# Kernel tuning notes

Measured on AMD Instinct MI355X. Metric: run time of the kernel, lower is better.

Reference implementation:

```python
import jax, jax.numpy as jnp
import numpy as np

IMG_H, IMG_W = 800, 1344
STRIDE = 16
FH, FW = IMG_H // STRIDE, IMG_W // STRIDE  # 50, 84
C = 1024
N_PROP = 3000
K_KEEP = 512          # post-NMS proposals kept by merge_proposals
POOL = 14             # C4 ROI-align output resolution
NMS_THRESH = 0.7
NUM_CLASSES = 80


def _make_boxes(key, n):
    r = jax.random.uniform(key, (n, 4))
    cx = r[:, 0] * IMG_W
    cy = r[:, 1] * IMG_H
    w = 16.0 + r[:, 2] * 480.0
    h = 16.0 + r[:, 3] * 480.0
    x0 = jnp.clip(cx - w / 2, 0.0, IMG_W)
    y0 = jnp.clip(cy - h / 2, 0.0, IMG_H)
    x1 = jnp.clip(cx + w / 2, 0.0, IMG_W)
    y1 = jnp.clip(cy + h / 2, 0.0, IMG_H)
    return jnp.stack([x0, y0, x1, y1], axis=-1)


def setup_inputs() -> dict:
    key = jax.random.key(0)
    ks = jax.random.split(key, 14)
    feat = jax.random.normal(ks[0], (C, FH, FW), jnp.float32)
    boxes1 = _make_boxes(ks[1], N_PROP)
    boxes2 = _make_boxes(ks[2], N_PROP)
    logits1 = jax.random.normal(ks[3], (N_PROP,), jnp.float32)
    logits2 = jax.random.normal(ks[4], (N_PROP,), jnp.float32)
    levels1 = jnp.zeros((N_PROP,), jnp.int32)  # single C4 level
    levels2 = jnp.zeros((N_PROP,), jnp.int32)
    scale1 = 1.0 + 0.02 * jax.random.normal(ks[5], (C,), jnp.float32)
    bias1 = 0.02 * jax.random.normal(ks[6], (C,), jnp.float32)
    scale2 = 1.0 + 0.02 * jax.random.normal(ks[7], (C,), jnp.float32)
    bias2 = 0.02 * jax.random.normal(ks[8], (C,), jnp.float32)
    W_cls1 = 0.01 * jax.random.normal(ks[9], (C, NUM_CLASSES + 1), jnp.float32)
    b_cls1 = jnp.zeros((NUM_CLASSES + 1,), jnp.float32)
    W_box1 = 0.001 * jax.random.normal(ks[10], (C, NUM_CLASSES * 4), jnp.float32)
    b_box1 = jnp.zeros((NUM_CLASSES * 4,), jnp.float32)
    W_cls2 = 0.01 * jax.random.normal(ks[11], (C, NUM_CLASSES + 1), jnp.float32)
    b_cls2 = jnp.zeros((NUM_CLASSES + 1,), jnp.float32)
    W_box2 = 0.001 * jax.random.normal(ks[12], (C, NUM_CLASSES * 4), jnp.float32)
    b_box2 = jnp.zeros((NUM_CLASSES * 4,), jnp.float32)
    return dict(feat=feat, boxes1=boxes1, boxes2=boxes2, logits1=logits1,
                logits2=logits2, levels1=levels1, levels2=levels2,
                scale1=scale1, bias1=bias1, scale2=scale2, bias2=bias2,
                W_cls1=W_cls1, b_cls1=b_cls1, W_box1=W_box1, b_box1=b_box1,
                W_cls2=W_cls2, b_cls2=b_cls2, W_box2=W_box2, b_box2=b_box2)


def _clip_boxes(boxes):
    return jnp.stack([jnp.clip(boxes[:, 0], 0.0, IMG_W),
                      jnp.clip(boxes[:, 1], 0.0, IMG_H),
                      jnp.clip(boxes[:, 2], 0.0, IMG_W),
                      jnp.clip(boxes[:, 3], 0.0, IMG_H)], axis=-1)


def _nms(boxes, scores, k, thresh):
    """Greedy NMS; returns k kept indices (fixed-size, jit-friendly)."""
    areas = (boxes[:, 2] - boxes[:, 0]) * (boxes[:, 3] - boxes[:, 1])

    def body(i, state):
        sw, keep = state
        idx = jnp.argmax(sw)
        keep = keep.at[i].set(idx.astype(jnp.int32))
        b = boxes[idx]
        ix0 = jnp.maximum(b[0], boxes[:, 0])
        iy0 = jnp.maximum(b[1], boxes[:, 1])
        ix1 = jnp.minimum(b[2], boxes[:, 2])
        iy1 = jnp.minimum(b[3], boxes[:, 3])
        inter = jnp.maximum(ix1 - ix0, 0.0) * jnp.maximum(iy1 - iy0, 0.0)
        iou = inter / (areas[idx] + areas - inter + 1e-9)
        sw = jnp.where(iou > thresh, -jnp.inf, sw)
        sw = sw.at[idx].set(-jnp.inf)
        return sw, keep

    keep0 = jnp.zeros((k,), jnp.int32)
    _, keep = jax.lax.fori_loop(0, k, body, (scores, keep0))
    return keep


def _roi_align(feat, boxes, spatial_scale, pool):
    """ROIAlign (aligned=True, sampling_ratio=1). feat [C,H,W], boxes [R,4] -> [R,C,pool,pool]."""
    Cc, H, W = feat.shape
    b = boxes * spatial_scale - 0.5
    x0, y0, x1, y1 = b[:, 0], b[:, 1], b[:, 2], b[:, 3]
    bw = (x1 - x0) / pool
    bh = (y1 - y0) / pool
    grid = jnp.arange(pool, dtype=feat.dtype) + 0.5
    xs = x0[:, None] + grid[None, :] * bw[:, None]  # [R,P]
    ys = y0[:, None] + grid[None, :] * bh[:, None]  # [R,P]
    yf = jnp.floor(ys); xf = jnp.floor(xs)
    ly = ys - yf; lx = xs - xf
    y0c = jnp.clip(yf.astype(jnp.int32), 0, H - 1)
    y1c = jnp.clip(yf.astype(jnp.int32) + 1, 0, H - 1)
    x0c = jnp.clip(xf.astype(jnp.int32), 0, W - 1)
    x1c = jnp.clip(xf.astype(jnp.int32) + 1, 0, W - 1)

    def g(Y, X):  # gather -> [C,R,P,P]
        return feat[:, Y[:, :, None], X[:, None, :]]

    wy0 = (1.0 - ly); wy1 = ly  # [R,P]
    wx0 = (1.0 - lx); wx1 = lx
    out = (g(y0c, x0c) * (wy0[:, :, None] * wx0[:, None, :])
           + g(y0c, x1c) * (wy0[:, :, None] * wx1[:, None, :])
           + g(y1c, x0c) * (wy1[:, :, None] * wx0[:, None, :])
           + g(y1c, x1c) * (wy1[:, :, None] * wx1[:, None, :]))
    return jnp.transpose(out, (1, 0, 2, 3))  # [R,C,P,P]


def _box_head(roi_feats, scale, bias, W_cls, b_cls, W_box, b_box):
    bf = roi_feats * scale[None, :, None, None] + bias[None, :, None, None]
    x = bf.mean(axis=(2, 3))  # [R,C]
    return bf, x @ W_cls + b_cls, x @ W_box + b_box


def reference(feat, boxes1, boxes2, logits1, logits2, levels1, levels2,
              scale1, bias1, scale2, bias2,
              W_cls1, b_cls1, W_box1, b_box1,
              W_cls2, b_cls2, W_box2, b_box2):
    boxes = _clip_boxes(jnp.concatenate([boxes1, boxes2], axis=0))
    scores = jnp.concatenate([logits1, logits2], axis=0)
    levels = jnp.concatenate([levels1, levels2], axis=0)
    # batched_nms level-offset trick (all zeros for single C4 level)
    off = levels.astype(boxes.dtype)[:, None] * float(max(IMG_H, IMG_W) + 1)
    keep = _nms(boxes + off, scores, K_KEEP, NMS_THRESH)
    prop = boxes[keep]  # [K,4] merged proposals

    roi = _roi_align(feat, prop, 1.0 / STRIDE, POOL)  # [K,C,P,P]
    bf1, s1, d1 = _box_head(roi, scale1, bias1, W_cls1, b_cls1, W_box1, b_box1)
    bf2, s2, d2 = _box_head(roi, scale2, bias2, W_cls2, b_cls2, W_box2, b_box2)
    return (bf1, bf2, s1, s2, d1, prop, feat)
```

## Files before the change

kernel.cpp:

```cpp
#include <hip/hip_runtime.h>

#define FHH 50
#define FWW 84
#define HW 4200
#define NBOX 6000
#define NPAD 6144
#define KKEEP 512
#define WSTRIDE 192

#define OFF_BF1  0ULL
#define OFF_BF2  102760448ULL
#define OFF_S1   205520896ULL
#define OFF_S2   205562368ULL
#define OFF_D1   205603840ULL
#define OFF_PROP 205767680ULL
#define OFF_FEAT 205769728ULL

__global__ __launch_bounds__(256) void k_transpose(const float* __restrict__ feat,
                                                   float* __restrict__ featT,
                                                   float* __restrict__ out_feat) {
  __shared__ float t[32][33];
  int hw0 = blockIdx.x * 32;
  int c0  = blockIdx.y * 32;
  int tx = threadIdx.x & 31, ty = threadIdx.x >> 5;
#pragma unroll
  for (int p = 0; p < 4; ++p) {
    int c = c0 + ty + p * 8;
    int hw = hw0 + tx;
    if (hw < HW) {
      float v = feat[(size_t)c * HW + hw];
      t[ty + p * 8][tx] = v;
      out_feat[(size_t)c * HW + hw] = v;
    }
  }
  __syncthreads();
#pragma unroll
  for (int p = 0; p < 4; ++p) {
    int hw = hw0 + ty + p * 8;
    int c = c0 + tx;
    if (hw < HW) featT[((size_t)hw << 10) + c] = t[tx][ty + p * 8];
  }
}

__global__ __launch_bounds__(256) void k_prep(const float4* __restrict__ boxes1,
                                              const float4* __restrict__ boxes2,
                                              const float* __restrict__ logits1,
                                              const float* __restrict__ logits2,
                                              const int* __restrict__ levels1,
                                              const int* __restrict__ levels2,
                                              float4* __restrict__ nbox,
                                              float* __restrict__ area,
                                              unsigned long long* __restrict__ keys,
                                              int* __restrict__ rank) {
  int i = blockIdx.x * 256 + threadIdx.x;
  if (i >= NPAD) return;
  if (i >= NBOX) { keys[i] = 0ULL; return; }
  rank[i] = 0;
  float4 b; float sc; int lv;
  if (i < 3000) { b = boxes1[i]; sc = logits1[i]; lv = levels1[i]; }
  else          { b = boxes2[i - 3000]; sc = logits2[i - 3000]; lv = levels2[i - 3000]; }
  float x0 = fminf(fmaxf(b.x, 0.f), 1344.f);
  float y0 = fminf(fmaxf(b.y, 0.f), 800.f);
  float x1 = fminf(fmaxf(b.z, 0.f), 1344.f);
  float y1 = fminf(fmaxf(b.w, 0.f), 800.f);
  float off = __fmul_rn((float)lv, 1345.0f);
  x0 = __fadd_rn(x0, off); y0 = __fadd_rn(y0, off);
  x1 = __fadd_rn(x1, off); y1 = __fadd_rn(y1, off);
  nbox[i] = make_float4(x0, y0, x1, y1);
  area[i] = __fmul_rn(__fsub_rn(x1, x0), __fsub_rn(y1, y0));
  unsigned u = __float_as_uint(sc);
  u = (u & 0x80000000u) ? ~u : (u | 0x80000000u);
  keys[i] = ((unsigned long long)u << 32) | (unsigned)(0xFFFFFFFFu - (unsigned)i);
}

__global__ __launch_bounds__(256) void k_rank(const unsigned long long* __restrict__ keys,
                                              int* __restrict__ rank) {
  __shared__ unsigned long long ks[1024];
  int jb = blockIdx.y;
  for (int t = threadIdx.x; t < 1024; t += 256) ks[t] = keys[jb * 1024 + t];
  __syncthreads();
  int i = blockIdx.x * 256 + threadIdx.x;
  if (i >= NBOX) return;
  unsigned long long ki = keys[i];
  int c = 0;
  for (int j = 0; j < 1024; ++j) c += (ks[j] > ki) ? 1 : 0;
  if (c) atomicAdd(&rank[i], c);
}

__global__ __launch_bounds__(256) void k_scatter(const float4* __restrict__ nbox,
                                                 const float* __restrict__ area,
                                                 const int* __restrict__ rank,
                                                 float4* __restrict__ sboxes,
                                                 float* __restrict__ sarea,
                                                 int* __restrict__ sorig) {
  int i = blockIdx.x * 256 + threadIdx.x;
  if (i >= NBOX) return;
  int r = rank[i];
  sboxes[r] = nbox[i];
  sarea[r] = area[i];
  sorig[r] = i;
}

__global__ __launch_bounds__(192) void k_mask(const float4* __restrict__ sboxes,
                                              const float* __restrict__ sarea,
                                              unsigned* __restrict__ mask) {
  int i0 = blockIdx.x * 4;
  int w = threadIdx.x;
  float4 b0 = sboxes[i0 + 0], b1 = sboxes[i0 + 1], b2 = sboxes[i0 + 2], b3 = sboxes[i0 + 3];
  float a0 = sarea[i0 + 0], a1 = sarea[i0 + 1], a2 = sarea[i0 + 2], a3 = sarea[i0 + 3];
  unsigned m0 = 0, m1 = 0, m2 = 0, m3 = 0;
  int jbase = w * 32;
  for (int bb = 0; bb < 32; ++bb) {
    int j = jbase + bb;
    if (j >= NBOX) break;
    float4 bj = sboxes[j];
    float aj = sarea[j];
#define IOU_BIT(BR, AR, MR)                                                          \
    {                                                                                \
      float ix0 = fmaxf(BR.x, bj.x), iy0 = fmaxf(BR.y, bj.y);                        \
      float ix1 = fminf(BR.z, bj.z), iy1 = fminf(BR.w, bj.w);                        \
      float iw = fmaxf(__fsub_rn(ix1, ix0), 0.f), ih = fmaxf(__fsub_rn(iy1, iy0), 0.f); \
      float inter = __fmul_rn(iw, ih);                                               \
      float den = __fadd_rn(__fsub_rn(__fadd_rn(AR, aj), inter), 1e-9f);             \
      float iou = __fdiv_rn(inter, den);                                             \
      if (iou > 0.7f) MR |= (1u << bb);                                              \
    }
    IOU_BIT(b0, a0, m0) IOU_BIT(b1, a1, m1) IOU_BIT(b2, a2, m2) IOU_BIT(b3, a3, m3)
#undef IOU_BIT
  }
  mask[(size_t)(i0 + 0) * WSTRIDE + w] = m0;
  mask[(size_t)(i0 + 1) * WSTRIDE + w] = m1;
  mask[(size_t)(i0 + 2) * WSTRIDE + w] = m2;
  mask[(size_t)(i0 + 3) * WSTRIDE + w] = m3;
}

#define SCAN_CH 64
__global__ __launch_bounds__(256) void k_scan(const unsigned* __restrict__ mask,
                                              const int* __restrict__ sorig,
                                              int* __restrict__ keep) {
  __shared__ unsigned srows[SCAN_CH * WSTRIDE];
  __shared__ unsigned rem[WSTRIDE];
  __shared__ int s_sorig[SCAN_CH];
  __shared__ int s_done;
  int tid = threadIdx.x;
  for (int i = tid; i < WSTRIDE; i += 256) rem[i] = 0;
  if (tid == 0) s_done = 0;
  __syncthreads();
  int kept = 0;
  for (int g = 0; g < 94; ++g) {
    int base = g * SCAN_CH;
    size_t gbase = (size_t)base * WSTRIDE;
    for (int idx = tid; idx < SCAN_CH * WSTRIDE; idx += 256) {
      size_t gi = gbase + idx;
      srows[idx] = (gi < (size_t)NBOX * WSTRIDE) ? mask[gi] : 0u;
    }
    if (tid < SCAN_CH) {
      int i = base + tid;
      s_sorig[tid] = (i < NBOX) ? sorig[i] : 0;
    }
    __syncthreads();
    if (tid < 64) {
      int lane = tid;
      for (int ww = 0; ww < 2; ++ww) {
        int w = (base >> 5) + ww;
        int wbase = w * 32;
        unsigned valid;
        int nv = NBOX - wbase;
        valid = (nv <= 0) ? 0u : (nv >= 32 ? 0xFFFFFFFFu : ((1u << nv) - 1u));
        unsigned rw = rem[w];
        unsigned avail = ~rw & valid;
        while (avail && kept < KKEEP) {
          int b = __builtin_ctz(avail);
          int i = wbase + b;
          int rr = i - base;
          if (lane == 0) keep[kept] = s_sorig[rr];
          kept++;
          rem[lane]       |= srows[rr * WSTRIDE + lane];
          rem[64 + lane]  |= srows[rr * WSTRIDE + 64 + lane];
          rem[128 + lane] |= srows[rr * WSTRIDE + 128 + lane];
          rw = rem[w];
          unsigned gt = (b == 31) ? 0u : ~((2u << b) - 1u);
          avail = ~rw & valid & gt;
        }
        if (kept >= KKEEP) break;
      }
      if (lane == 0 && kept >= KKEEP) s_done = 1;
    }
    __syncthreads();
    if (s_done) break;
  }
  if (tid < 64) {
    for (int k = kept + tid; k < KKEEP; k += 64) keep[k] = 0;
  }
}

__global__ __launch_bounds__(256) void k_prop(const int* __restrict__ keep,
                                              const float4* __restrict__ boxes1,
                                              const float4* __restrict__ boxes2,
                                              float4* __restrict__ prop) {
  int k = blockIdx.x * 256 + threadIdx.x;
  if (k >= KKEEP) return;
  int o = keep[k];
  float4 b = (o < 3000) ? boxes1[o] : boxes2[o - 3000];
  prop[k] = make_float4(fminf(fmaxf(b.x, 0.f), 1344.f),
                        fminf(fmaxf(b.y, 0.f), 800.f),
                        fminf(fmaxf(b.z, 0.f), 1344.f),
                        fminf(fmaxf(b.w, 0.f), 800.f));
}

__global__ __launch_bounds__(256) void k_bilin(const float4* __restrict__ prop,
                                               float4* __restrict__ bilinW,
                                               int4* __restrict__ bilinA) {
  int r = blockIdx.x;
  int bin = threadIdx.x;
  if (bin >= 196) return;
  float4 pb = prop[r];
  const float ss = 0.0625f;
  float x0s = pb.x * ss - 0.5f, y0s = pb.y * ss - 0.5f;
  float bw = (pb.z * ss - 0.5f - x0s) / 14.0f;
  float bh = (pb.w * ss - 0.5f - y0s) / 14.0f;
  int py = bin / 14, px = bin - py * 14;
  float xs = x0s + ((float)px + 0.5f) * bw;
  float ys = y0s + ((float)py + 0.5f) * bh;
  float xf = floorf(xs), yf = floorf(ys);
  float lx = xs - xf, ly = ys - yf;
  int ix = (int)xf, iy = (int)yf;
  int x0c = min(max(ix, 0), FWW - 1), x1c = min(max(ix + 1, 0), FWW - 1);
  int y0c = min(max(iy, 0), FHH - 1), y1c = min(max(iy + 1, 0), FHH - 1);
  float wy0 = 1.f - ly, wx0 = 1.f - lx;
  bilinW[r * 196 + bin] = make_float4(wy0 * wx0, wy0 * lx, ly * wx0, ly * lx);
  bilinA[r * 196 + bin] = make_int4((y0c * FWW + x0c) << 10, (y0c * FWW + x1c) << 10,
                                    (y1c * FWW + x0c) << 10, (y1c * FWW + x1c) << 10);
}

__global__ __launch_bounds__(256) void k_roi(const float* __restrict__ featT,
                                             const float4* __restrict__ bilinW,
                                             const int4* __restrict__ bilinA,
                                             const float* __restrict__ scale1,
                                             const float* __restrict__ bias1,
                                             const float* __restrict__ scale2,
                                             const float* __restrict__ bias2,
                                             float* __restrict__ bf1,
                                             float* __restrict__ bf2,
                                             float* __restrict__ x1w,
                                             float* __restrict__ x2w) {
  __shared__ float tile[64 * 197];
  __shared__ float part2f[4 * 64];
  __shared__ float sc1[64], bi1[64], sc2[64], bi2[64];
  int bid = blockIdx.x;
  int r = (bid & 7) + ((bid >> 7) << 3);
  int c0 = ((bid >> 3) & 15) * 64;
  int tid = threadIdx.x;
  int l16 = tid & 15, bg = tid >> 4;
  if (tid < 64) {
    sc1[tid] = scale1[c0 + tid]; bi1[tid] = bias1[c0 + tid];
    sc2[tid] = scale2[c0 + tid]; bi2[tid] = bias2[c0 + tid];
  }
  const float* fTb = featT + c0 + l16 * 4;
  const float4* bW = bilinW + r * 196;
  const int4* bA = bilinA + r * 196;
  float4 acc = make_float4(0.f, 0.f, 0.f, 0.f);

#define ROI_BODY(BB)                                                              \
  {                                                                               \
    float4 w = bW[BB]; int4 a = bA[BB];                                           \
    float4 g00 = *(const float4*)(fTb + a.x);                                     \
    float4 g01 = *(const float4*)(fTb + a.y);                                     \
    float4 g10 = *(const float4*)(fTb + a.z);                                     \
    float4 g11 = *(const float4*)(fTb + a.w);                                     \
    float vx = g00.x * w.x + g01.x * w.y + g10.x * w.z + g11.x * w.w;             \
    float vy = g00.y * w.x + g01.y * w.y + g10.y * w.z + g11.y * w.w;             \
    float vz = g00.z * w.x + g01.z * w.y + g10.z * w.z + g11.z * w.w;             \
    float vw = g00.w * w.x + g01.w * w.y + g10.w * w.z + g11.w * w.w;             \
    acc.x += vx; acc.y += vy; acc.z += vz; acc.w += vw;                           \
    int tb = l16 * 788 + (BB);                                                    \
    tile[tb] = vx; tile[tb + 197] = vy; tile[tb + 394] = vz; tile[tb + 591] = vw; \
  }

  int bb = bg;
#pragma unroll 4
  for (int i = 0; i < 12; ++i, bb += 16) ROI_BODY(bb)
  if (bg < 4) ROI_BODY(192 + bg)
#undef ROI_BODY

  acc.x += __shfl_xor(acc.x, 16); acc.y += __shfl_xor(acc.y, 16);
  acc.z += __shfl_xor(acc.z, 16); acc.w += __shfl_xor(acc.w, 16);
  acc.x += __shfl_xor(acc.x, 32); acc.y += __shfl_xor(acc.y, 32);
  acc.z += __shfl_xor(acc.z, 32); acc.w += __shfl_xor(acc.w, 32);
  if ((tid & 63) < 16) {
    int wv = tid >> 6;
    part2f[wv * 64 + l16 * 4 + 0] = acc.x;
    part2f[wv * 64 + l16 * 4 + 1] = acc.y;
    part2f[wv * 64 + l16 * 4 + 2] = acc.z;
    part2f[wv * 64 + l16 * 4 + 3] = acc.w;
  }
  __syncthreads();
  if (tid < 64) {
    float m = ((part2f[tid] + part2f[64 + tid]) + part2f[128 + tid]) + part2f[192 + tid];
    m = m / 196.0f;
    x1w[((size_t)r << 10) + c0 + tid] = m * sc1[tid] + bi1[tid];
    x2w[((size_t)r << 10) + c0 + tid] = m * sc2[tid] + bi2[tid];
  }
  size_t ob = ((size_t)((r << 10) + c0)) * 196;
  for (int it = 0; it < 49; ++it) {
    int flat = tid + it * 256;
    unsigned cl = (unsigned)flat / 196u;
    int bin = flat - (int)cl * 196;
    float v = tile[cl * 197 + bin];
    bf1[ob + flat] = v * sc1[cl] + bi1[cl];
    bf2[ob + flat] = v * sc2[cl] + bi2[cl];
  }
}

__global__ __launch_bounds__(256) void k_gemm(const float* __restrict__ x1,
                                              const float* __restrict__ x2,
                                              const float* __restrict__ Wc1, const float* __restrict__ bc1,
                                              const float* __restrict__ Wb1, const float* __restrict__ bb1,
                                              const float* __restrict__ Wc2, const float* __restrict__ bc2,
                                              float* __restrict__ s1, float* __restrict__ d1,
                                              float* __restrict__ s2) {
  int z = blockIdx.z;
  const float* A; const float* W; const float* bias; float* out; int N;
  if (z == 0)      { A = x1; W = Wc1; bias = bc1; out = s1; N = 81; }
  else if (z == 1) { A = x1; W = Wb1; bias = bb1; out = d1; N = 320; }
  else             { A = x2; W = Wc2; bias = bc2; out = s2; N = 81; }
  int n0 = blockIdx.y * 32;
  if (n0 >= N) return;
  int m0 = blockIdx.x * 32;
  __shared__ float As[32][34];
  __shared__ float Bs[32][34];
  int tid = threadIdx.x;
  int tx = tid & 15, ty = tid >> 4;
  float acc00 = 0, acc01 = 0, acc10 = 0, acc11 = 0;
  for (int k0 = 0; k0 < 1024; k0 += 32) {
    int mm = tid >> 3, g = tid & 7;
    float4 av = *(const float4*)(A + (size_t)(m0 + mm) * 1024 + k0 + g * 4);
    As[g * 4 + 0][mm] = av.x; As[g * 4 + 1][mm] = av.y;
    As[g * 4 + 2][mm] = av.z; As[g * 4 + 3][mm] = av.w;
    int nn = tid & 31, kh = tid >> 5;
#pragma unroll
    for (int qq = 0; qq < 4; ++qq) {
      int kk = kh + 8 * qq;
      int n = n0 + nn;
      Bs[kk][nn] = (n < N) ? W[(size_t)(k0 + kk) * N + n] : 0.f;
    }
    __syncthreads();
#pragma unroll
    for (int kk = 0; kk < 32; ++kk) {
      float2 a = *(const float2*)&As[kk][2 * ty];
      float2 b = *(const float2*)&Bs[kk][2 * tx];
      acc00 += a.x * b.x; acc01 += a.x * b.y;
      acc10 += a.y * b.x; acc11 += a.y * b.y;
    }
    __syncthreads();
  }
  int m = m0 + 2 * ty, n = n0 + 2 * tx;
  if (n < N) {
    out[(size_t)m * N + n] = acc00 + bias[n];
    out[(size_t)(m + 1) * N + n] = acc10 + bias[n];
  }
  if (n + 1 < N) {
    out[(size_t)m * N + n + 1] = acc01 + bias[n + 1];
    out[(size_t)(m + 1) * N + n + 1] = acc11 + bias[n + 1];
  }
}

extern "C" void kernel_launch(void* const* d_in, const int* in_sizes, int n_in,
                              void* d_out, int out_size, void* d_ws, size_t ws_size,
                              hipStream_t stream) {
  (void)in_sizes; (void)n_in; (void)out_size; (void)ws_size;
  const float* feat    = (const float*)d_in[0];
  const float4* boxes1 = (const float4*)d_in[1];
  const float4* boxes2 = (const float4*)d_in[2];
  const float* logits1 = (const float*)d_in[3];
  const float* logits2 = (const float*)d_in[4];
  const int* levels1   = (const int*)d_in[5];
  const int* levels2   = (const int*)d_in[6];
  const float* scale1  = (const float*)d_in[7];
  const float* bias1   = (const float*)d_in[8];
  const float* scale2  = (const float*)d_in[9];
  const float* bias2   = (const float*)d_in[10];
  const float* W_cls1  = (const float*)d_in[11];
  const float* b_cls1  = (const float*)d_in[12];
  const float* W_box1  = (const float*)d_in[13];
  const float* b_box1  = (const float*)d_in[14];
  const float* W_cls2  = (const float*)d_in[15];
  const float* b_cls2  = (const float*)d_in[16];

  float* out = (float*)d_out;
  char* w = (char*)d_ws;
  float* featT              = (float*)(w + 0);
  unsigned long long* keys  = (unsigned long long*)(w + 17203200);
  float4* nbox              = (float4*)(w + 17252352);
  float* area               = (float*)(w + 17348352);
  int* rank                 = (int*)(w + 17372352);
  float4* sboxes            = (float4*)(w + 17396352);
  float* sarea              = (float*)(w + 17492352);
  int* sorig                = (int*)(w + 17516352);
  unsigned* mask            = (unsigned*)(w + 17540352);
  int* keep                 = (int*)(w + 22148352);
  float* x1w                = (float*)(w + 22150400);
  float* x2w                = (float*)(w + 24247552);
  float4* bilinW            = (float4*)(w + 17540352);
  int4* bilinA              = (int4*)(w + 19145984);

  k_transpose<<<dim3(132, 32), 256, 0, stream>>>(feat, featT, out + OFF_FEAT);
  k_prep<<<24, 256, 0, stream>>>(boxes1, boxes2, logits1, logits2, levels1, levels2,
                                 nbox, area, keys, rank);
  k_rank<<<dim3(24, 6), 256, 0, stream>>>(keys, rank);
  k_scatter<<<24, 256, 0, stream>>>(nbox, area, rank, sboxes, sarea, sorig);
  k_mask<<<1500, 192, 0, stream>>>(sboxes, sarea, mask);
  k_scan<<<1, 256, 0, stream>>>(mask, sorig, keep);
  k_prop<<<2, 256, 0, stream>>>(keep, boxes1, boxes2, (float4*)(out + OFF_PROP));
  k_bilin<<<512, 256, 0, stream>>>((const float4*)(out + OFF_PROP), bilinW, bilinA);
  k_roi<<<8192, 256, 0, stream>>>(featT, bilinW, bilinA,
                                  scale1, bias1, scale2, bias2,
                                  out + OFF_BF1, out + OFF_BF2, x1w, x2w);
  k_gemm<<<dim3(16, 10, 3), 256, 0, stream>>>(x1w, x2w, W_cls1, b_cls1, W_box1, b_box1,
                                              W_cls2, b_cls2,
                                              out + OFF_S1, out + OFF_D1, out + OFF_S2);
}
```

Measured before the change: 575.3 us.

## Double-buffer NMS scan with register-held removal mask; vectorize nontemporal output stores

The NMS scan kernel now prefetches the next chunk of mask rows into a second shared buffer using the spare warps, while warp 0 walks the rows sequentially. The removal mask is kept in registers and read back through shuffles instead of shared memory, so the block-wide load/sync stall per chunk goes away. Separately, the big bf1/bf2 writes are emitted as 2-wide nontemporal stores, and the feat copy uses nontemporal stores, to cut cache pollution and store instruction count. The scan now visits every row rather than skipping suppressed ones via ctz, which adds a per-row shuffle.

```diff
diff --git a/kernel.cpp b/kernel.cpp
--- a/kernel.cpp
+++ b/kernel.cpp
@@ -7,6 +7,8 @@
 #define NPAD 6144
 #define KKEEP 512
 #define WSTRIDE 192
+
+typedef float f32x2 __attribute__((ext_vector_type(2)));
 
 #define OFF_BF1  0ULL
 #define OFF_BF2  102760448ULL
@@ -30,7 +32,7 @@
     if (hw < HW) {
       float v = feat[(size_t)c * HW + hw];
       t[ty + p * 8][tx] = v;
-      out_feat[(size_t)c * HW + hw] = v;
+      __builtin_nontemporal_store(v, &out_feat[(size_t)c * HW + hw]);
     }
   }
   __syncthreads();
@@ -138,60 +140,63 @@
 __global__ __launch_bounds__(256) void k_scan(const unsigned* __restrict__ mask,
                                               const int* __restrict__ sorig,
                                               int* __restrict__ keep) {
-  __shared__ unsigned srows[SCAN_CH * WSTRIDE];
-  __shared__ unsigned rem[WSTRIDE];
-  __shared__ int s_sorig[SCAN_CH];
-  __shared__ int s_done;
+  __shared__ unsigned srows[2][SCAN_CH * WSTRIDE];
+  __shared__ int s_sorig[2][SCAN_CH];
+  __shared__ int s_done, s_kept;
   int tid = threadIdx.x;
-  for (int i = tid; i < WSTRIDE; i += 256) rem[i] = 0;
-  if (tid == 0) s_done = 0;
+  if (tid == 0) { s_done = 0; s_kept = 0; }
+  for (int idx = tid; idx < SCAN_CH * WSTRIDE; idx += 256) srows[0][idx] = mask[idx];
+  if (tid < SCAN_CH) s_sorig[0][tid] = sorig[tid];
   __syncthreads();
+  unsigned r0 = 0, r1 = 0, r2 = 0;
+  int lane = tid;
   int kept = 0;
   for (int g = 0; g < 94; ++g) {
-    int base = g * SCAN_CH;
-    size_t gbase = (size_t)base * WSTRIDE;
-    for (int idx = tid; idx < SCAN_CH * WSTRIDE; idx += 256) {
-      size_t gi = gbase + idx;
-      srows[idx] = (gi < (size_t)NBOX * WSTRIDE) ? mask[gi] : 0u;
-    }
-    if (tid < SCAN_CH) {
-      int i = base + tid;
-      s_sorig[tid] = (i < NBOX) ? sorig[i] : 0;
-    }
-    __syncthreads();
-    if (tid < 64) {
-      int lane = tid;
-      for (int ww = 0; ww < 2; ++ww) {
-        int w = (base >> 5) + ww;
-        int wbase = w * 32;
-        unsigned valid;
-        int nv = NBOX - wbase;
-        valid = (nv <= 0) ? 0u : (nv >= 32 ? 0xFFFFFFFFu : ((1u << nv) - 1u));
-        unsigned rw = rem[w];
-        unsigned avail = ~rw & valid;
-        while (avail && kept < KKEEP) {
-          int b = __builtin_ctz(avail);
-          int i = wbase + b;
-          int rr = i - base;
-          if (lane == 0) keep[kept] = s_sorig[rr];
+    int cur = g & 1, nxt = cur ^ 1;
+    if (tid >= 64) {
+      int gn = g + 1;
+      if (gn < 94) {
+        size_t gbase = (size_t)gn * SCAN_CH * WSTRIDE;
+        for (int idx = tid - 64; idx < SCAN_CH * WSTRIDE; idx += 192) {
+          size_t gi = gbase + idx;
+          srows[nxt][idx] = (gi < (size_t)NBOX * WSTRIDE) ? mask[gi] : 0u;
+        }
+        if (tid - 64 < SCAN_CH) {
+          int i2 = gn * SCAN_CH + (tid - 64);
+          s_sorig[nxt][tid - 64] = (i2 < NBOX) ? sorig[i2] : 0;
+        }
+      }
+    } else {
+      int base = g * SCAN_CH;
+      int nrows = min(SCAN_CH, NBOX - base);
+      const unsigned* sb = srows[cur];
+      unsigned p0 = sb[lane], p1 = sb[64 + lane], p2 = sb[128 + lane];
+      for (int rr = 0; rr < nrows; ++rr) {
+        unsigned c0v = p0, c1v = p1, c2v = p2;
+        int rn = (rr + 1 < nrows) ? rr + 1 : rr;
+        p0 = sb[rn * WSTRIDE + lane];
+        p1 = sb[rn * WSTRIDE + 64 + lane];
+        p2 = sb[rn * WSTRIDE + 128 + lane];
+        int i = base + rr;
+        int w = i >> 5, b = i & 31;
+        int wl = w & 63, wc = w >> 6;
+        unsigned rsel = (wc == 0) ? r0 : ((wc == 1) ? r1 : r2);
+        unsigned rw = __shfl(rsel, wl);
+        if (!((rw >> b) & 1u)) {
+          r0 |= c0v; r1 |= c1v; r2 |= c2v;
+          if (lane == 0) keep[kept] = s_sorig[cur][rr];
           kept++;
-          rem[lane]       |= srows[rr * WSTRIDE + lane];
-          rem[64 + lane]  |= srows[rr * WSTRIDE + 64 + lane];
-          rem[128 + lane] |= srows[rr * WSTRIDE + 128 + lane];
-          rw = rem[w];
-          unsigned gt = (b == 31) ? 0u : ~((2u << b) - 1u);
-          avail = ~rw & valid & gt;
+          if (kept >= KKEEP) break;
         }
-        if (kept >= KKEEP) break;
       }
-      if (lane == 0 && kept >= KKEEP) s_done = 1;
+      if (lane == 0) { s_kept = kept; if (kept >= KKEEP) s_done = 1; }
     }
     __syncthreads();
     if (s_done) break;
   }
-  if (tid < 64) {
-    for (int k = kept + tid; k < KKEEP; k += 64) keep[k] = 0;
-  }
+  __syncthreads();
+  int fk = s_kept;
+  for (int k = fk + tid; k < KKEEP; k += 256) keep[k] = 0;
 }
 
 __global__ __launch_bounds__(256) void k_prop(const int* __restrict__ keep,
@@ -302,13 +307,21 @@
     x2w[((size_t)r << 10) + c0 + tid] = m * sc2[tid] + bi2[tid];
   }
   size_t ob = ((size_t)((r << 10) + c0)) * 196;
-  for (int it = 0; it < 49; ++it) {
-    int flat = tid + it * 256;
-    unsigned cl = (unsigned)flat / 196u;
-    int bin = flat - (int)cl * 196;
-    float v = tile[cl * 197 + bin];
-    bf1[ob + flat] = v * sc1[cl] + bi1[cl];
-    bf2[ob + flat] = v * sc2[cl] + bi2[cl];
+  float* b1p = bf1 + ob;
+  float* b2p = bf2 + ob;
+  for (int it = 0; it < 25; ++it) {
+    int f2 = tid + it * 256;
+    if (f2 < 6272) {
+      int cl = (int)((unsigned)f2 / 98u);
+      int bin = (f2 - cl * 98) * 2;
+      int tb = cl * 197 + bin;
+      float v0 = tile[tb], v1 = tile[tb + 1];
+      float s1v = sc1[cl], b1v = bi1[cl], s2v = sc2[cl], b2v = bi2[cl];
+      f32x2 o1 = { v0 * s1v + b1v, v1 * s1v + b1v };
+      f32x2 o2 = { v0 * s2v + b2v, v1 * s2v + b2v };
+      __builtin_nontemporal_store(o1, (f32x2*)(b1p + 2 * f2));
+      __builtin_nontemporal_store(o2, (f32x2*)(b2p + 2 * f2));
+    }
   }
 }
 
```

Measured after the change: 483.0 us. 1.19x faster.
